# Performance work log

Hardware: AMD Instinct MI355X
Metric: run time of the kernel (lower is better)

Reference implementation:

```python
import jax, jax.numpy as jnp
import numpy as np

B, S, H, L = 4096, 64, 768, 5
TEMP = 0.07
BN_EPS = 1e-5


def setup_inputs() -> dict:
    key = jax.random.key(0)
    ks = jax.random.split(key, 8)
    seq = jax.random.normal(ks[0], (B, S, H), dtype=jnp.float32)
    labels = jax.random.randint(ks[1], (B,), 0, L)
    s = 1.0 / np.sqrt(H)
    return {
        'sequence_output': seq,
        'cls_gamma': jnp.ones((H,), jnp.float32),
        'cls_beta': jnp.zeros((H,), jnp.float32),
        'cls_W': jax.random.normal(ks[2], (H, H), jnp.float32) * s,
        'cls_b': jax.random.normal(ks[3], (H,), jnp.float32) * 0.01,
        'label_gamma': jnp.ones((H,), jnp.float32),
        'label_beta': jnp.zeros((H,), jnp.float32),
        'label_W': jax.random.normal(ks[4], (H, H), jnp.float32) * s,
        'label_b': jax.random.normal(ks[5], (H,), jnp.float32) * 0.01,
        'labels': labels,
    }


def _batchnorm(x, gamma, beta):
    # training-mode BatchNorm1d: biased batch stats
    m = x.mean(0)
    v = jnp.mean((x - m) ** 2, axis=0)
    return (x - m) * jax.lax.rsqrt(v + BN_EPS) * gamma + beta


def _l2norm(x):
    return x / jnp.sqrt(jnp.sum(x * x, axis=-1, keepdims=True)).clip(1e-12)


def reference(sequence_output, cls_gamma, cls_beta, cls_W, cls_b,
              label_gamma, label_beta, label_W, label_b, labels):
    z = sequence_output[:, 0, :]  # [B,H]; dropout is identity in eval
    # label token spans: 'No relation' -> positions 1:3 (mean), rest single tokens 3..6
    theta = jnp.stack([
        sequence_output[:, 1:3, :].mean(axis=1),
        sequence_output[:, 3, :],
        sequence_output[:, 4, :],
        sequence_output[:, 5, :],
        sequence_output[:, 6, :],
    ], axis=1)  # [B,L,H]
    z_cl, theta_cl = z, theta

    zp = _batchnorm(z, cls_gamma, cls_beta) @ cls_W.T + cls_b  # [B,H]
    tp = _batchnorm(theta.reshape(-1, H), label_gamma, label_beta) @ label_W.T + label_b
    tp = tp.reshape(-1, L, H)  # [B,L,H]
    logits = jnp.einsum('blh,bh->bl', tp, zp)  # [B,L]

    # ---- dual supervised contrastive loss (vectorized over the python loops) ----
    z_norm = _l2norm(z_cl)        # [B,H]
    theta_norm = _l2norm(theta_cl)  # [B,L,H]
    same = labels[:, None] == labels[None, :]          # [B,B]
    eye = jnp.eye(labels.shape[0], dtype=bool)
    pos_mask = (same & ~eye).astype(jnp.float32)       # positives (same label, j != i)
    neg_mask = (~same).astype(jnp.float32)             # negatives (different label)
    has_pos = (same & ~eye).any(axis=1)

    # l_z: anchor z_i vs theta_j[labels_i] (pos) and all theta_j[:] for diff-label j (neg)
    expS = jnp.exp(jnp.einsum('ih,jlh->ijl', z_norm, theta_norm) / TEMP)  # [B,B,L]
    expS_at_lab = jnp.take_along_axis(
        expS, jnp.broadcast_to(labels[:, None, None], expS.shape[:2] + (1,)), axis=2
    )[..., 0]  # expS[i,j,labels[i]] -> [B,B]
    pos_z = jnp.sum(expS_at_lab * pos_mask, axis=1)
    neg_z = jnp.sum(expS.sum(axis=-1) * neg_mask, axis=1)
    l_z = jnp.where(has_pos, -jnp.log(pos_z / (pos_z + neg_z + 1e-8)), 0.0).sum()

    # l_theta: anchor theta_i[labels_i] vs z_j
    anchor_theta = jnp.take_along_axis(theta_norm, labels[:, None, None], axis=1)[:, 0, :]  # [B,H]
    expT = jnp.exp(anchor_theta @ z_norm.T / TEMP)  # [B,B]
    pos_t = jnp.sum(expT * pos_mask, axis=1)
    neg_t = jnp.sum(expT * neg_mask, axis=1)
    l_t = jnp.where(has_pos, -jnp.log(pos_t / (pos_t + neg_t + 1e-8)), 0.0).sum()

    dual_loss = (l_z + l_t) / labels.shape[0]
    return logits, dual_loss
```

## Files before the change

kernel.cpp:

```cpp
#include <hip/hip_runtime.h>
#include <hip/hip_bf16.h>
#include <cstdint>
#include <cstddef>

#define B_N 4096
#define S_N 64
#define H_N 768
#define L_N 5
#define TEMP_INV (1.0f / 0.07f)
#define BN_EPS 1e-5f

typedef __attribute__((ext_vector_type(8))) short short8;
typedef __attribute__((ext_vector_type(4))) float f32x4;

__device__ __forceinline__ void async_copy16(void* lds, const void* g) {
  __builtin_amdgcn_global_load_lds(
      (const __attribute__((address_space(1))) unsigned int*)g,
      (__attribute__((address_space(3))) unsigned int*)lds, 16, 0, 0);
}

__device__ __forceinline__ unsigned short bf16b(float x) {
  __hip_bfloat16 h = __float2bfloat16(x);
  return *reinterpret_cast<unsigned short*>(&h);
}
__device__ __forceinline__ void store_bf16x4(void* p, float4 v) {
  ushort4 o = make_ushort4(bf16b(v.x), bf16b(v.y), bf16b(v.z), bf16b(v.w));
  *reinterpret_cast<ushort4*>(p) = o;
}

__device__ inline float block_reduce_sum256(float v, float* sbuf) {
#pragma unroll
  for (int off = 32; off > 0; off >>= 1) v += __shfl_down(v, off, 64);
  int lane = threadIdx.x & 63;
  int wid = threadIdx.x >> 6;
  __syncthreads();
  if (lane == 0) sbuf[wid] = v;
  __syncthreads();
  float r = 0.f;
  if (threadIdx.x == 0) r = sbuf[0] + sbuf[1] + sbuf[2] + sbuf[3];
  return r;
}

__global__ __launch_bounds__(256) void extract_kernel(
    const float* __restrict__ seq, __hip_bfloat16* __restrict__ zb,
    __hip_bfloat16* __restrict__ tb, float* __restrict__ zn_inv,
    float* __restrict__ thn_inv, float* __restrict__ sum_z,
    float* __restrict__ ssq_z, float* __restrict__ sum_t,
    float* __restrict__ ssq_t) {
  __shared__ float pr[16][6][3];
  int t = threadIdx.x;
  int wv = t >> 6, ln = t & 63;
  bool act = t < 192;
  int c4 = t * 4;
  int b0 = blockIdx.x * 16;
  float zs[4] = {}, zq[4] = {}, ts4[4] = {}, tq4[4] = {};
  for (int r = 0; r < 16; ++r) {
    int b = b0 + r;
    const float* base = seq + (size_t)b * (S_N * H_N);
    float pv[6] = {0.f, 0.f, 0.f, 0.f, 0.f, 0.f};
    if (act) {
      float4 z4 = *(const float4*)(base + c4);
      store_bf16x4(zb + (size_t)b * H_N + c4, z4);
      pv[0] = z4.x * z4.x + z4.y * z4.y + z4.z * z4.z + z4.w * z4.w;
      zs[0] += z4.x; zs[1] += z4.y; zs[2] += z4.z; zs[3] += z4.w;
      zq[0] += z4.x * z4.x; zq[1] += z4.y * z4.y;
      zq[2] += z4.z * z4.z; zq[3] += z4.w * z4.w;
#pragma unroll
      for (int l = 0; l < L_N; ++l) {
        float4 v4;
        if (l == 0) {
          float4 a4 = *(const float4*)(base + H_N + c4);
          float4 b4 = *(const float4*)(base + 2 * H_N + c4);
          v4 = make_float4(0.5f * (a4.x + b4.x), 0.5f * (a4.y + b4.y),
                           0.5f * (a4.z + b4.z), 0.5f * (a4.w + b4.w));
        } else {
          v4 = *(const float4*)(base + (size_t)(l + 2) * H_N + c4);
        }
        store_bf16x4(tb + ((size_t)b * L_N + l) * H_N + c4, v4);
        pv[1 + l] = v4.x * v4.x + v4.y * v4.y + v4.z * v4.z + v4.w * v4.w;
        ts4[0] += v4.x; ts4[1] += v4.y; ts4[2] += v4.z; ts4[3] += v4.w;
        tq4[0] += v4.x * v4.x; tq4[1] += v4.y * v4.y;
        tq4[2] += v4.z * v4.z; tq4[3] += v4.w * v4.w;
      }
    }
#pragma unroll
    for (int v = 0; v < 6; ++v) {
      float x = pv[v];
#pragma unroll
      for (int off = 32; off > 0; off >>= 1) x += __shfl_down(x, off, 64);
      if (ln == 0 && wv < 3) pr[r][v][wv] = x;
    }
  }
  __syncthreads();
  if (t < 96) {
    int r = t / 6, v = t - r * 6;
    float s = pr[r][v][0] + pr[r][v][1] + pr[r][v][2];
    float inv = 1.f / fmaxf(sqrtf(s), 1e-12f);
    int b = b0 + r;
    if (v == 0) zn_inv[b] = inv;
    else thn_inv[b * L_N + (v - 1)] = inv;
  }
  if (act) {
#pragma unroll
    for (int j = 0; j < 4; ++j) {
      atomicAdd(&sum_z[c4 + j], zs[j]);
      atomicAdd(&ssq_z[c4 + j], zq[j]);
      atomicAdd(&sum_t[c4 + j], ts4[j]);
      atomicAdd(&ssq_t[c4 + j], tq4[j]);
    }
  }
}

__global__ void count_kernel(const int* __restrict__ labels, int* __restrict__ cnt) {
  int i = blockIdx.x * 256 + threadIdx.x;
  if (i < B_N) atomicAdd(&cnt[labels[i]], 1);
}

__global__ void finalize_kernel(
    const float* __restrict__ sum_z, const float* __restrict__ ssq_z,
    const float* __restrict__ sum_t, const float* __restrict__ ssq_t,
    const float* __restrict__ g_z, const float* __restrict__ b_z,
    const float* __restrict__ g_t, const float* __restrict__ b_t,
    float* __restrict__ sz_s, float* __restrict__ sz_t,
    float* __restrict__ st_s, float* __restrict__ st_t) {
  int h = blockIdx.x * 256 + threadIdx.x;
  if (h >= H_N) return;
  {
    float m = sum_z[h] * (1.f / B_N);
    float v = ssq_z[h] * (1.f / B_N) - m * m;
    float s = g_z[h] * rsqrtf(v + BN_EPS);
    sz_s[h] = s;
    sz_t[h] = b_z[h] - m * s;
  }
  {
    float m = sum_t[h] * (1.f / (B_N * L_N));
    float v = ssq_t[h] * (1.f / (B_N * L_N)) - m * m;
    float s = g_t[h] * rsqrtf(v + BN_EPS);
    st_s[h] = s;
    st_t[h] = b_t[h] - m * s;
  }
}

__global__ __launch_bounds__(256) void prep_cls_kernel(
    const float* __restrict__ W, const float* __restrict__ szs,
    const float* __restrict__ szt, const float* __restrict__ bias,
    __hip_bfloat16* __restrict__ Wb, float* __restrict__ cprime) {
  __shared__ float sbuf[4];
  int n = blockIdx.x;
  int t = threadIdx.x;
  float dot = 0.f;
  if (t < 192) {
    int c4 = t * 4;
    const float* row = W + (size_t)n * H_N;
    float4 w4 = *(const float4*)(row + c4);
    float4 s4 = *(const float4*)(szs + c4);
    float4 t4 = *(const float4*)(szt + c4);
    store_bf16x4(Wb + (size_t)n * H_N + c4,
                 make_float4(w4.x * s4.x, w4.y * s4.y, w4.z * s4.z, w4.w * s4.w));
    dot = w4.x * t4.x + w4.y * t4.y + w4.z * t4.z + w4.w * t4.w;
  }
  float s = block_reduce_sum256(dot, sbuf);
  if (t == 0) cprime[n] = s + bias[n];
}

__global__ __launch_bounds__(256) void transpose_wl_kernel(
    const float* __restrict__ Wl, __hip_bfloat16* __restrict__ WlT) {
  __shared__ float tile[32][33];
  int t = threadIdx.x;
  int tx = t & 31, ty0 = t >> 5;
  int n0 = blockIdx.x * 32, k0 = blockIdx.y * 32;
#pragma unroll
  for (int p = 0; p < 4; ++p)
    tile[ty0 + p * 8][tx] = Wl[(size_t)(n0 + ty0 + p * 8) * H_N + k0 + tx];
  __syncthreads();
#pragma unroll
  for (int p = 0; p < 4; ++p) {
    unsigned short us = bf16b(tile[tx][ty0 + p * 8]);
    *((unsigned short*)WlT + (size_t)(k0 + ty0 + p * 8) * H_N + n0 + tx) = us;
  }
}

template <bool WRITE_BF16, bool HAS_BIAS>
__global__ __launch_bounds__(256) void gemm128_kernel(
    const __hip_bfloat16* __restrict__ A, const __hip_bfloat16* __restrict__ Bm,
    const float* __restrict__ bias, float* __restrict__ outF,
    __hip_bfloat16* __restrict__ outB) {
  __shared__ __align__(16) __hip_bfloat16 Asm[128 * 32];
  __shared__ __align__(16) __hip_bfloat16 Bsm[128 * 32];
  int tid = threadIdx.x, lane = tid & 63, wid = tid >> 6;
  int wr = wid >> 1, wc = wid & 1;
  int i0 = blockIdx.x * 128, n0 = blockIdx.y * 128;
  int llo = lane & 15, lhi = lane >> 4;
  f32x4 acc[4][4] = {};
  for (int k0 = 0; k0 < H_N; k0 += 32) {
#pragma unroll
    for (int r = 0; r < 2; ++r) {
      int s = r * 256 + wid * 64 + lane;
      int row = s >> 2, kc = (s & 3) * 8;
      size_t go = (size_t)row * H_N + k0 + kc;
      async_copy16((char*)Asm + (size_t)(r * 256 + wid * 64) * 16,
                   A + (size_t)i0 * H_N + go);
      async_copy16((char*)Bsm + (size_t)(r * 256 + wid * 64) * 16,
                   Bm + (size_t)n0 * H_N + go);
    }
    __syncthreads();
    short8 a[4], b[4];
#pragma unroll
    for (int m = 0; m < 4; ++m)
      a[m] = *(const short8*)((const char*)Asm +
                              ((wr * 64 + m * 16 + llo) * 32 + lhi * 8) * 2);
#pragma unroll
    for (int n = 0; n < 4; ++n)
      b[n] = *(const short8*)((const char*)Bsm +
                              ((wc * 64 + n * 16 + llo) * 32 + lhi * 8) * 2);
#pragma unroll
    for (int m = 0; m < 4; ++m)
#pragma unroll
      for (int n = 0; n < 4; ++n)
        acc[m][n] =
            __builtin_amdgcn_mfma_f32_16x16x32_bf16(a[m], b[n], acc[m][n], 0, 0, 0);
    __syncthreads();
  }
#pragma unroll
  for (int n = 0; n < 4; ++n) {
    int col = n0 + wc * 64 + n * 16 + llo;
    float bv = HAS_BIAS ? bias[col] : 0.f;
#pragma unroll
    for (int m = 0; m < 4; ++m) {
#pragma unroll
      for (int r = 0; r < 4; ++r) {
        int row = i0 + wr * 64 + m * 16 + lhi * 4 + r;
        float val = acc[m][n][r] + bv;
        outF[(size_t)row * H_N + col] = val;
        if (WRITE_BF16)
          outB[(size_t)row * H_N + col] = __float2bfloat16(val);
      }
    }
  }
}

__global__ __launch_bounds__(256) void logits_kernel(
    const float* __restrict__ seq, const float* __restrict__ u,
    const float* __restrict__ zp, const float* __restrict__ st_s,
    const float* __restrict__ st_t, const float* __restrict__ label_b,
    float* __restrict__ out) {
  __shared__ float sbuf[4];
  int b = blockIdx.x;
  int t = threadIdx.x;
  bool act = t < 192;
  int c4 = t * 4;
  float4 w4 = make_float4(0.f, 0.f, 0.f, 0.f);
  float apart = 0.f;
  if (act) {
    float4 u4 = *(const float4*)(u + (size_t)b * H_N + c4);
    float4 zp4 = *(const float4*)(zp + (size_t)b * H_N + c4);
    float4 ss4 = *(const float4*)(st_s + c4);
    float4 tt4 = *(const float4*)(st_t + c4);
    float4 lb4 = *(const float4*)(label_b + c4);
    w4 = make_float4(u4.x * ss4.x, u4.y * ss4.y, u4.z * ss4.z, u4.w * ss4.w);
    apart = u4.x * tt4.x + u4.y * tt4.y + u4.z * tt4.z + u4.w * tt4.w +
            zp4.x * lb4.x + zp4.y * lb4.y + zp4.z * lb4.z + zp4.w * lb4.w;
  }
  float alpha = block_reduce_sum256(apart, sbuf);
  const float* base = seq + (size_t)b * (S_N * H_N);
#pragma unroll
  for (int l = 0; l < L_N; ++l) {
    float part = 0.f;
    if (act) {
      float4 v4;
      if (l == 0) {
        float4 a4 = *(const float4*)(base + H_N + c4);
        float4 b4 = *(const float4*)(base + 2 * H_N + c4);
        v4 = make_float4(0.5f * (a4.x + b4.x), 0.5f * (a4.y + b4.y),
                         0.5f * (a4.z + b4.z), 0.5f * (a4.w + b4.w));
      } else {
        v4 = *(const float4*)(base + (size_t)(l + 2) * H_N + c4);
      }
      part = v4.x * w4.x + v4.y * w4.y + v4.z * w4.z + v4.w * w4.w;
    }
    float s = block_reduce_sum256(part, sbuf);
    if (t == 0) out[b * L_N + l] = s + alpha;
  }
}

#define NT_K 12
__global__ __launch_bounds__(512, 1) void sgemm_fused_kernel(
    const __hip_bfloat16* __restrict__ zb, const __hip_bfloat16* __restrict__ tb,
    const float* __restrict__ zn_inv, const float* __restrict__ thn_inv,
    const int* __restrict__ labels, float* __restrict__ pos_z,
    float* __restrict__ neg_z, float* __restrict__ pos_t,
    float* __restrict__ neg_t) {
  __shared__ __align__(128) char ldsbuf[2][65536];

  const int tid = threadIdx.x;
  const int lane = tid & 63, wid = tid >> 6;
  const int llo = lane & 15, lhi = lane >> 4;
  const int wrbase = (wid >> 2) * 128;
  const int wcbase = (wid & 3) * 64;
  const int i0 = blockIdx.x * 256, n0 = blockIdx.y * 256;

  f32x4 acc[8][4] = {};

  auto stagePart = [&](int c, int kt, int p) {
    int s = p * 512 + tid;
    int row = s >> 3;
    int lq = (s & 7) ^ (row & 7);
    int kofs = kt * 64 + lq * 8;
    int wub = (p * 512 + wid * 64) * 16;
    async_copy16(&ldsbuf[c][0] + wub, zb + (size_t)(i0 + row) * H_N + kofs);
    async_copy16(&ldsbuf[c][32768] + wub, tb + (size_t)(n0 + row) * H_N + kofs);
  };

#pragma unroll
  for (int p = 0; p < 4; ++p) stagePart(0, 0, p);
  asm volatile("s_waitcnt vmcnt(0)" ::: "memory");
  __builtin_amdgcn_s_barrier();

  for (int t = 0; t < NT_K; ++t) {
    const char* ldsA = &ldsbuf[t & 1][0];
    const char* ldsB = &ldsbuf[t & 1][32768];
#pragma unroll
    for (int p = 0; p < 4; ++p) {
      const int kk = p >> 1, mh = (p & 1) * 4;
      const int slot = ((kk * 4 + lhi) ^ (llo & 7)) * 16;
      short8 a[4], b[4];
#pragma unroll
      for (int m = 0; m < 4; ++m) {
        int row = wrbase + (mh + m) * 16 + llo;
        a[m] = *(const short8*)(ldsA + row * 128 + slot);
      }
#pragma unroll
      for (int n = 0; n < 4; ++n) {
        int col = wcbase + n * 16 + llo;
        b[n] = *(const short8*)(ldsB + col * 128 + slot);
      }
      if (t + 1 < NT_K) stagePart((t + 1) & 1, t + 1, p);
      __builtin_amdgcn_s_barrier();
      asm volatile("s_waitcnt lgkmcnt(0)" ::: "memory");
      __builtin_amdgcn_sched_barrier(0);
      __builtin_amdgcn_s_setprio(1);
#pragma unroll
      for (int m = 0; m < 4; ++m)
#pragma unroll
        for (int n = 0; n < 4; ++n)
          acc[mh + m][n] = __builtin_amdgcn_mfma_f32_16x16x32_bf16(
              a[m], b[n], acc[mh + m][n], 0, 0, 0);
      __builtin_amdgcn_s_setprio(0);
      if (p == 3)
        asm volatile("s_waitcnt vmcnt(0)" ::: "memory");
      __builtin_amdgcn_s_barrier();
    }
  }
  __syncthreads();

  float* rpos = (float*)&ldsbuf[0][0];
  float* rneg = rpos + 256;
  float* cpos = rneg + 256;
  float* cneg = cpos + 256;
  float* rnorm = cneg + 256;
  float* cnorm = rnorm + 256;
  int* rowlab = (int*)(cnorm + 256);
  int* colj = rowlab + 256;
  int* coll = colj + 256;
  int* collab = coll + 256;

  if (tid < 256) {
    rowlab[tid] = labels[i0 + tid];
    rnorm[tid] = zn_inv[i0 + tid] * TEMP_INV;
    int c = n0 + tid;
    int j = c / 5;
    colj[tid] = j;
    coll[tid] = c - j * 5;
    collab[tid] = labels[j];
    cnorm[tid] = thn_inv[c];
    rpos[tid] = 0.f; rneg[tid] = 0.f; cpos[tid] = 0.f; cneg[tid] = 0.f;
  }
  __syncthreads();

  int cl[4], jg[4], lv[4], lj[4];
  float cs[4];
#pragma unroll
  for (int ni = 0; ni < 4; ++ni) {
    cl[ni] = wcbase + ni * 16 + llo;
    jg[ni] = colj[cl[ni]];
    lv[ni] = coll[cl[ni]];
    lj[ni] = collab[cl[ni]];
    cs[ni] = cnorm[cl[ni]];
  }
  float cpAcc[4] = {}, cnAcc[4] = {};
#pragma unroll
  for (int mi = 0; mi < 8; ++mi) {
#pragma unroll
    for (int r = 0; r < 4; ++r) {
      int rl = wrbase + mi * 16 + lhi * 4 + r;
      int ig = i0 + rl;
      int li = rowlab[rl];
      float rscale = rnorm[rl];
      float rp = 0.f, rn = 0.f;
#pragma unroll
      for (int ni = 0; ni < 4; ++ni) {
        float e = __expf(acc[mi][ni][r] * rscale * cs[ni]);
        bool same = (li == lj[ni]);
        bool diag = (ig == jg[ni]);
        if (same) {
          if (!diag && lv[ni] == li) { rp += e; cpAcc[ni] += e; }
        } else {
          rn += e;
          if (lv[ni] == lj[ni]) cnAcc[ni] += e;
        }
      }
      if (rp != 0.f) atomicAdd(&rpos[rl], rp);
      if (rn != 0.f) atomicAdd(&rneg[rl], rn);
    }
  }
#pragma unroll
  for (int ni = 0; ni < 4; ++ni) {
    if (cpAcc[ni] != 0.f) atomicAdd(&cpos[cl[ni]], cpAcc[ni]);
    if (cnAcc[ni] != 0.f) atomicAdd(&cneg[cl[ni]], cnAcc[ni]);
  }
  __syncthreads();
  if (tid < 256) {
    float v;
    v = rpos[tid]; if (v != 0.f) atomicAdd(&pos_z[i0 + tid], v);
    v = rneg[tid]; if (v != 0.f) atomicAdd(&neg_z[i0 + tid], v);
    int j = colj[tid];
    v = cpos[tid]; if (v != 0.f) atomicAdd(&pos_t[j], v);
    v = cneg[tid]; if (v != 0.f) atomicAdd(&neg_t[j], v);
  }
}

__global__ __launch_bounds__(256) void loss_kernel(
    const float* __restrict__ pos_z, const float* __restrict__ neg_z,
    const float* __restrict__ pos_t, const float* __restrict__ neg_t,
    const int* __restrict__ labels, const int* __restrict__ cnt,
    float* __restrict__ out_loss) {
  __shared__ float sbuf[4];
  int i = blockIdx.x * 256 + threadIdx.x;
  float term = 0.f;
  int li = labels[i];
  if (cnt[li] > 1) {
    float pz = pos_z[i], nz = neg_z[i];
    float pt = pos_t[i], nt = neg_t[i];
    term = -logf(pz / (pz + nz + 1e-8f)) - logf(pt / (pt + nt + 1e-8f));
  }
  float s = block_reduce_sum256(term, sbuf);
  if (threadIdx.x == 0) atomicAdd(out_loss, s * (1.0f / B_N));
}

extern "C" void kernel_launch(void* const* d_in, const int* in_sizes, int n_in,
                              void* d_out, int out_size, void* d_ws, size_t ws_size,
                              hipStream_t stream) {
  const float* seq = (const float*)d_in[0];
  const float* cls_gamma = (const float*)d_in[1];
  const float* cls_beta = (const float*)d_in[2];
  const float* cls_W = (const float*)d_in[3];
  const float* cls_b = (const float*)d_in[4];
  const float* label_gamma = (const float*)d_in[5];
  const float* label_beta = (const float*)d_in[6];
  const float* label_W = (const float*)d_in[7];
  const float* label_b = (const float*)d_in[8];
  const int* labels = (const int*)d_in[9];
  float* out = (float*)d_out;
  float* ws = (float*)d_ws;

  constexpr size_t OFF_SUMZ = 0;
  constexpr size_t OFF_SSQZ = 768;
  constexpr size_t OFF_SUMT = 1536;
  constexpr size_t OFF_SSQT = 2304;
  constexpr size_t OFF_POSZ = 3072;
  constexpr size_t OFF_NEGZ = 7168;
  constexpr size_t OFF_POST = 11264;
  constexpr size_t OFF_NEGT = 15360;
  constexpr size_t OFF_CNT = 19456;
  constexpr size_t ZERO_FLOATS = 19464;
  constexpr size_t OFF_SZS = 19464;
  constexpr size_t OFF_SZT = 20232;
  constexpr size_t OFF_STS = 21000;
  constexpr size_t OFF_STT = 21768;
  constexpr size_t OFF_ZNI = 22536;
  constexpr size_t OFF_TNI = 26632;
  constexpr size_t OFF_CPRIME = 47112;
  constexpr size_t OFF_ZP = 47880;
  constexpr size_t OFF_U = OFF_ZP + (size_t)B_N * H_N;
  constexpr size_t F32_END = OFF_U + (size_t)B_N * H_N;
  constexpr size_t BYTE_ZB = F32_END * sizeof(float);
  constexpr size_t BYTE_TB = BYTE_ZB + (size_t)B_N * H_N * 2;
  constexpr size_t BYTE_ZPB = BYTE_TB + (size_t)B_N * L_N * H_N * 2;
  constexpr size_t BYTE_WCB = BYTE_ZPB + (size_t)B_N * H_N * 2;
  constexpr size_t BYTE_WLT = BYTE_WCB + (size_t)H_N * H_N * 2;
  constexpr size_t TOTAL_BYTES = BYTE_WLT + (size_t)H_N * H_N * 2;
  if (ws_size < TOTAL_BYTES) return;

  __hip_bfloat16* zb = (__hip_bfloat16*)((char*)d_ws + BYTE_ZB);
  __hip_bfloat16* tb = (__hip_bfloat16*)((char*)d_ws + BYTE_TB);
  __hip_bfloat16* zpb = (__hip_bfloat16*)((char*)d_ws + BYTE_ZPB);
  __hip_bfloat16* wcb = (__hip_bfloat16*)((char*)d_ws + BYTE_WCB);
  __hip_bfloat16* wlt = (__hip_bfloat16*)((char*)d_ws + BYTE_WLT);

  hipMemsetAsync(d_ws, 0, ZERO_FLOATS * sizeof(float), stream);
  hipMemsetAsync((char*)d_out + (size_t)B_N * L_N * sizeof(float), 0, sizeof(float),
                 stream);

  extract_kernel<<<256, 256, 0, stream>>>(seq, zb, tb, ws + OFF_ZNI, ws + OFF_TNI,
                                          ws + OFF_SUMZ, ws + OFF_SSQZ,
                                          ws + OFF_SUMT, ws + OFF_SSQT);
  count_kernel<<<16, 256, 0, stream>>>(labels, (int*)(ws + OFF_CNT));
  finalize_kernel<<<3, 256, 0, stream>>>(
      ws + OFF_SUMZ, ws + OFF_SSQZ, ws + OFF_SUMT, ws + OFF_SSQT, cls_gamma,
      cls_beta, label_gamma, label_beta, ws + OFF_SZS, ws + OFF_SZT, ws + OFF_STS,
      ws + OFF_STT);
  prep_cls_kernel<<<H_N, 256, 0, stream>>>(cls_W, ws + OFF_SZS, ws + OFF_SZT, cls_b,
                                           wcb, ws + OFF_CPRIME);
  transpose_wl_kernel<<<dim3(24, 24), 256, 0, stream>>>(label_W, wlt);
  gemm128_kernel<true, true><<<dim3(32, 6), 256, 0, stream>>>(
      zb, wcb, ws + OFF_CPRIME, ws + OFF_ZP, zpb);
  gemm128_kernel<false, false><<<dim3(32, 6), 256, 0, stream>>>(
      zpb, wlt, nullptr, ws + OFF_U, nullptr);
  logits_kernel<<<B_N, 256, 0, stream>>>(seq, ws + OFF_U, ws + OFF_ZP, ws + OFF_STS,
                                         ws + OFF_STT, label_b, out);
  sgemm_fused_kernel<<<dim3(16, 80), 512, 0, stream>>>(
      zb, tb, ws + OFF_ZNI, ws + OFF_TNI, labels, ws + OFF_POSZ, ws + OFF_NEGZ,
      ws + OFF_POST, ws + OFF_NEGT);
  loss_kernel<<<16, 256, 0, stream>>>(ws + OFF_POSZ, ws + OFF_NEGZ, ws + OFF_POST,
                                      ws + OFF_NEGT, labels,
                                      (const int*)(ws + OFF_CNT),
                                      out + (size_t)B_N * L_N);
}
```

Before: 455.9 us.

## Deepen sgemm pipeline to 4 LDS stages with K=32 tiles; double extract grid

The contrastive sgemm kernel drops from two 64-wide K stages to four 32-wide K stages. It prefetches two tiles ahead with vmcnt(4) waits and uses a new XOR swizzle for the 64-byte rows. The aim is to hide global-load latency better, at the cost of twice as many barriers per K. The extract kernel also handles 8 rows per block instead of 16, doubling its grid for more parallelism but adding more atomics to the BN stats.

```diff
diff --git a/kernel.cpp b/kernel.cpp
--- a/kernel.cpp
+++ b/kernel.cpp
@@ -47,14 +47,14 @@
     float* __restrict__ thn_inv, float* __restrict__ sum_z,
     float* __restrict__ ssq_z, float* __restrict__ sum_t,
     float* __restrict__ ssq_t) {
-  __shared__ float pr[16][6][3];
+  __shared__ float pr[8][6][3];
   int t = threadIdx.x;
   int wv = t >> 6, ln = t & 63;
   bool act = t < 192;
   int c4 = t * 4;
-  int b0 = blockIdx.x * 16;
+  int b0 = blockIdx.x * 8;
   float zs[4] = {}, zq[4] = {}, ts4[4] = {}, tq4[4] = {};
-  for (int r = 0; r < 16; ++r) {
+  for (int r = 0; r < 8; ++r) {
     int b = b0 + r;
     const float* base = seq + (size_t)b * (S_N * H_N);
     float pv[6] = {0.f, 0.f, 0.f, 0.f, 0.f, 0.f};
@@ -92,7 +92,7 @@
     }
   }
   __syncthreads();
-  if (t < 96) {
+  if (t < 48) {
     int r = t / 6, v = t - r * 6;
     float s = pr[r][v][0] + pr[r][v][1] + pr[r][v][2];
     float inv = 1.f / fmaxf(sqrtf(s), 1e-12f);
@@ -283,14 +283,14 @@
   }
 }
 
-#define NT_K 12
+#define NT_K 24
 __global__ __launch_bounds__(512, 1) void sgemm_fused_kernel(
     const __hip_bfloat16* __restrict__ zb, const __hip_bfloat16* __restrict__ tb,
     const float* __restrict__ zn_inv, const float* __restrict__ thn_inv,
     const int* __restrict__ labels, float* __restrict__ pos_z,
     float* __restrict__ neg_z, float* __restrict__ pos_t,
     float* __restrict__ neg_t) {
-  __shared__ __align__(128) char ldsbuf[2][65536];
+  __shared__ __align__(128) char ldsbuf[4][32768];
 
   const int tid = threadIdx.x;
   const int lane = tid & 63, wid = tid >> 6;
@@ -301,40 +301,41 @@
 
   f32x4 acc[8][4] = {};
 
-  auto stagePart = [&](int c, int kt, int p) {
-    int s = p * 512 + tid;
-    int row = s >> 3;
-    int lq = (s & 7) ^ (row & 7);
-    int kofs = kt * 64 + lq * 8;
-    int wub = (p * 512 + wid * 64) * 16;
+  auto stageQ = [&](int c, int kt, int q) {
+    int s = q * 512 + tid;
+    int row = s >> 2;
+    int sl = s & 3;
+    int lq = sl ^ ((row ^ (row >> 2)) & 3);
+    int kofs = kt * 32 + lq * 8;
+    int wub = (q * 512 + wid * 64) * 16;
     async_copy16(&ldsbuf[c][0] + wub, zb + (size_t)(i0 + row) * H_N + kofs);
-    async_copy16(&ldsbuf[c][32768] + wub, tb + (size_t)(n0 + row) * H_N + kofs);
+    async_copy16(&ldsbuf[c][16384] + wub, tb + (size_t)(n0 + row) * H_N + kofs);
   };
 
-#pragma unroll
-  for (int p = 0; p < 4; ++p) stagePart(0, 0, p);
-  asm volatile("s_waitcnt vmcnt(0)" ::: "memory");
+  stageQ(0, 0, 0); stageQ(0, 0, 1);
+  stageQ(1, 1, 0); stageQ(1, 1, 1);
+  asm volatile("s_waitcnt vmcnt(4)" ::: "memory");
   __builtin_amdgcn_s_barrier();
 
   for (int t = 0; t < NT_K; ++t) {
-    const char* ldsA = &ldsbuf[t & 1][0];
-    const char* ldsB = &ldsbuf[t & 1][32768];
-#pragma unroll
-    for (int p = 0; p < 4; ++p) {
-      const int kk = p >> 1, mh = (p & 1) * 4;
-      const int slot = ((kk * 4 + lhi) ^ (llo & 7)) * 16;
+    const char* ldsA = &ldsbuf[t & 3][0];
+    const char* ldsB = &ldsbuf[t & 3][16384];
+#pragma unroll
+    for (int mh = 0; mh < 2; ++mh) {
       short8 a[4], b[4];
 #pragma unroll
       for (int m = 0; m < 4; ++m) {
-        int row = wrbase + (mh + m) * 16 + llo;
-        a[m] = *(const short8*)(ldsA + row * 128 + slot);
+        int row = wrbase + (mh * 4 + m) * 16 + llo;
+        a[m] = *(const short8*)(ldsA + row * 64 +
+                                ((lhi ^ ((row ^ (row >> 2)) & 3)) * 16));
       }
 #pragma unroll
       for (int n = 0; n < 4; ++n) {
         int col = wcbase + n * 16 + llo;
-        b[n] = *(const short8*)(ldsB + col * 128 + slot);
-      }
-      if (t + 1 < NT_K) stagePart((t + 1) & 1, t + 1, p);
+        b[n] = *(const short8*)(ldsB + col * 64 +
+                                ((lhi ^ ((col ^ (col >> 2)) & 3)) * 16));
+      }
+      if (t + 2 < NT_K) stageQ((t + 2) & 3, t + 2, mh);
       __builtin_amdgcn_s_barrier();
       asm volatile("s_waitcnt lgkmcnt(0)" ::: "memory");
       __builtin_amdgcn_sched_barrier(0);
@@ -343,11 +344,15 @@
       for (int m = 0; m < 4; ++m)
 #pragma unroll
         for (int n = 0; n < 4; ++n)
-          acc[mh + m][n] = __builtin_amdgcn_mfma_f32_16x16x32_bf16(
-              a[m], b[n], acc[mh + m][n], 0, 0, 0);
+          acc[mh * 4 + m][n] = __builtin_amdgcn_mfma_f32_16x16x32_bf16(
+              a[m], b[n], acc[mh * 4 + m][n], 0, 0, 0);
       __builtin_amdgcn_s_setprio(0);
-      if (p == 3)
-        asm volatile("s_waitcnt vmcnt(0)" ::: "memory");
+      if (mh == 1) {
+        if (t < NT_K - 2)
+          asm volatile("s_waitcnt vmcnt(4)" ::: "memory");
+        else
+          asm volatile("s_waitcnt vmcnt(0)" ::: "memory");
+      }
       __builtin_amdgcn_s_barrier();
     }
   }
@@ -501,7 +506,7 @@
   hipMemsetAsync((char*)d_out + (size_t)B_N * L_N * sizeof(float), 0, sizeof(float),
                  stream);
 
-  extract_kernel<<<256, 256, 0, stream>>>(seq, zb, tb, ws + OFF_ZNI, ws + OFF_TNI,
+  extract_kernel<<<512, 256, 0, stream>>>(seq, zb, tb, ws + OFF_ZNI, ws + OFF_TNI,
                                           ws + OFF_SUMZ, ws + OFF_SSQZ,
                                           ws + OFF_SUMT, ws + OFF_SSQT);
   count_kernel<<<16, 256, 0, stream>>>(labels, (int*)(ws + OFF_CNT));
```

Result: slower. 482.2 us (+5.8%).
